# Kernel optimization log

Hardware: AMD Instinct MI355X
Metric: run time of the kernel (lower is better)

## Reference

```python
import jax, jax.numpy as jnp
import numpy as np

NUM_HEADS = 16
H_DIM = 1024
HEAD_DIM = H_DIM // NUM_HEADS  # 64
B, S = 8, 1024


def setup_inputs() -> dict:
    key = jax.random.key(0)
    ks = jax.random.split(key, 8)
    query = jax.random.normal(ks[0], (B, S, H_DIM), dtype=jnp.float32)
    key_t = jax.random.normal(ks[1], (B, S, H_DIM), dtype=jnp.float32)
    value = jax.random.normal(ks[2], (B, S, H_DIM), dtype=jnp.float32)
    attn_mask = jnp.ones((B, S, S), dtype=jnp.int32)
    # Per-head projection weights, stacked: [H, h_dim, head_dim]
    sc = 1.0 / np.sqrt(H_DIM)
    Wq = jax.random.normal(ks[3], (NUM_HEADS, H_DIM, HEAD_DIM), dtype=jnp.float32) * sc
    Wk = jax.random.normal(ks[4], (NUM_HEADS, H_DIM, HEAD_DIM), dtype=jnp.float32) * sc
    Wv = jax.random.normal(ks[5], (NUM_HEADS, H_DIM, HEAD_DIM), dtype=jnp.float32) * sc
    Wo = jax.random.normal(ks[6], (H_DIM, H_DIM), dtype=jnp.float32) * sc
    return {"query": query, "key": key_t, "value": value, "attn_mask": attn_mask,
            "Wq": Wq, "Wk": Wk, "Wv": Wv, "Wo": Wo}


def reference(query, key, value, attn_mask, Wq, Wk, Wv, Wo):
    scale = 1.0 / jnp.sqrt(jnp.float32(HEAD_DIM))  # from DotProductAttention.build
    # Fused per-head projections: [B,S,D] x [H,D,K] -> [B,H,S,K]
    q = jnp.einsum('bsd,hdk->bhsk', query, Wq)
    k = jnp.einsum('bsd,hdk->bhsk', key, Wk)
    v = jnp.einsum('bsd,hdk->bhsk', value, Wv)
    # Scores [B,H,S,S]; masked_fill where mask==0 (applied before scaling,
    # matching original; -inf * scale stays -inf)
    score = jnp.einsum('bhqk,bhmk->bhqm', q, k)
    mask = attn_mask[:, None, :, :]  # broadcast over heads
    score = jnp.where(mask == 0, -jnp.inf, score)
    p = jax.nn.softmax(score * scale, axis=-1)
    head = jnp.einsum('bhqm,bhmk->bhqk', p, v)  # [B,H,S,K]
    # Concat heads along feature dim: [B,S,H*K]
    concat = head.transpose(0, 2, 1, 3).reshape(B, S, H_DIM)
    return concat @ Wo
```

## Files before the change

kernel.cpp:

```cpp
#include <hip/hip_runtime.h>
#include <stdint.h>


typedef unsigned short u16;
typedef __attribute__((ext_vector_type(8))) short bf16x8;
typedef __attribute__((ext_vector_type(4))) float f32x4;
typedef __attribute__((ext_vector_type(4))) short short4_t;

#define MFMA16(a, b, c) __builtin_amdgcn_mfma_f32_16x16x32_bf16((a), (b), (c), 0, 0, 0)

__device__ __forceinline__ u16 f2bf(float f) {
  union { float f; uint32_t u; } v; v.f = f;
  uint32_t r = v.u + 0x7fffu + ((v.u >> 16) & 1u);
  return (u16)(r >> 16);
}
__device__ __forceinline__ u16 f2bf_fast(float f) {
  union { float f; uint32_t u; } v; v.f = f;
  return (u16)((v.u + 0x8000u) >> 16);
}

__device__ __forceinline__ void async16(const void* g, void* l) {
  __builtin_amdgcn_global_load_lds(
      (const __attribute__((address_space(1))) void*)g,
      (__attribute__((address_space(3))) void*)l, 16, 0, 0);
}

__device__ __forceinline__ void gemm_core(u16* As, u16* Bs, const u16* A,
                                          const u16* Bt, u16* C, float* Cf,
                                          int m0, int n0, int mode) {
  const int tid = threadIdx.x;
  const int lane = tid & 63;
  const int w = tid >> 6;
  const int wm = w >> 1, wn = w & 1;
  const int m_l = lane & 15;
  const int quad = lane >> 4;

  f32x4 acc[4][4];
#pragma unroll
  for (int i = 0; i < 4; i++)
#pragma unroll
    for (int j = 0; j < 4; j++) acc[i][j] = (f32x4){0.f, 0.f, 0.f, 0.f};

  const int rB = lane >> 2;
  const int cB = (((lane & 3) ^ ((rB >> 1) & 3))) * 8;
  const u16* a0 = A + (size_t)(m0 + (2 * w + 0) * 16 + rB) * 1024 + cB;
  const u16* a1 = A + (size_t)(m0 + (2 * w + 1) * 16 + rB) * 1024 + cB;
  const u16* b0 = Bt + (size_t)(n0 + (2 * w + 0) * 16 + rB) * 1024 + cB;
  const u16* b1 = Bt + (size_t)(n0 + (2 * w + 1) * 16 + rB) * 1024 + cB;
  u16* as0 = &As[(2 * w + 0) * 512];
  u16* as1 = &As[(2 * w + 1) * 512];
  u16* bs0 = &Bs[(2 * w + 0) * 512];
  u16* bs1 = &Bs[(2 * w + 1) * 512];

  for (int k0 = 0; k0 < 1024; k0 += 32) {
    __syncthreads();
    async16(a0 + k0, as0);
    async16(a1 + k0, as1);
    async16(b0 + k0, bs0);
    async16(b1 + k0, bs1);
    __syncthreads();

    bf16x8 af[4], bfr[4];
#pragma unroll
    for (int mt = 0; mt < 4; mt++) {
      int row = wm * 64 + mt * 16 + m_l;
      af[mt] =
          *(const bf16x8*)&As[row * 32 + (quad ^ ((m_l >> 1) & 3)) * 8];
    }
#pragma unroll
    for (int nt = 0; nt < 4; nt++) {
      int row = wn * 64 + nt * 16 + m_l;
      bfr[nt] =
          *(const bf16x8*)&Bs[row * 32 + (quad ^ ((m_l >> 1) & 3)) * 8];
    }
#pragma unroll
    for (int mt = 0; mt < 4; mt++)
#pragma unroll
      for (int nt = 0; nt < 4; nt++)
        acc[mt][nt] = MFMA16(af[mt], bfr[nt], acc[mt][nt]);
  }

#pragma unroll
  for (int mt = 0; mt < 4; mt++) {
    int m_base = m0 + wm * 64 + mt * 16 + quad * 4;
    int b = m_base >> 10, s = m_base & 1023;
#pragma unroll
    for (int nt = 0; nt < 4; nt++) {
      int n_g = n0 + wn * 64 + nt * 16 + m_l;
      if (mode == 0) {
        int h = n_g >> 6, d = n_g & 63;
        u16* p = C + ((size_t)(b * 16 + h) * 1024 + s) * 64 + d;
#pragma unroll
        for (int r = 0; r < 4; r++) p[(size_t)r * 64] = f2bf(acc[mt][nt][r]);
      } else if (mode == 1) {
        int h = n_g >> 6, d = n_g & 63;
        u16* p = C + ((size_t)(b * 16 + h) * 64 + d) * 1024 + s;
        short4_t pk;
#pragma unroll
        for (int r = 0; r < 4; r++) pk[r] = (short)f2bf(acc[mt][nt][r]);
        *(short4_t*)p = pk;
      } else {
        float* p = Cf + (size_t)m_base * 1024 + n_g;
#pragma unroll
        for (int r = 0; r < 4; r++) p[(size_t)r * 1024] = acc[mt][nt][r];
      }
    }
  }
}

__global__ __launch_bounds__(256) void qkv_kernel(
    const u16* __restrict__ q, const u16* __restrict__ k,
    const u16* __restrict__ v, const u16* __restrict__ wtq,
    const u16* __restrict__ wtk, const u16* __restrict__ wtv, u16* qb,
    u16* kb, u16* vt) {
  __shared__ u16 As[128 * 32], Bs[128 * 32];
  int z = blockIdx.z;
  const u16* A = (z == 0) ? q : (z == 1) ? k : v;
  const u16* Bt = (z == 0) ? wtq : (z == 1) ? wtk : wtv;
  u16* C = (z == 0) ? qb : (z == 1) ? kb : vt;
  gemm_core(As, Bs, A, Bt, C, nullptr, blockIdx.x * 128, blockIdx.y * 128,
            (z == 2) ? 1 : 0);
}

__global__ __launch_bounds__(256) void out_kernel(const u16* __restrict__ cc,
                                                  const u16* __restrict__ wto,
                                                  float* out) {
  __shared__ u16 As[128 * 32], Bs[128 * 32];
  gemm_core(As, Bs, cc, wto, nullptr, out, blockIdx.x * 128,
            blockIdx.y * 128, 2);
}

__global__ void conv_kernel(const float* __restrict__ q,
                            const float* __restrict__ k,
                            const float* __restrict__ v, u16* qc, u16* kc,
                            u16* vc) {
  int z = blockIdx.y;
  size_t t = ((size_t)blockIdx.x * 256 + threadIdx.x) * 4;
  const float* src = (z == 0) ? q : (z == 1) ? k : v;
  u16* dst = (z == 0) ? qc : (z == 1) ? kc : vc;
  float4 f = *(const float4*)(src + t);
  short4_t o;
  o[0] = (short)f2bf(f.x);
  o[1] = (short)f2bf(f.y);
  o[2] = (short)f2bf(f.z);
  o[3] = (short)f2bf(f.w);
  *(short4_t*)(dst + t) = o;
}

__global__ __launch_bounds__(256) void repack_t_kernel(
    const float* __restrict__ Wq, const float* __restrict__ Wk,
    const float* __restrict__ Wv, u16* wtq, u16* wtk, u16* wtv) {
  __shared__ u16 Ts[64 * 66];
  const int h = blockIdx.x, kkt = blockIdx.y, z = blockIdx.z;
  const float* W = (z == 0) ? Wq : (z == 1) ? Wk : Wv;
  u16* O = (z == 0) ? wtq : (z == 1) ? wtk : wtv;
  const int w = threadIdx.x >> 6, lane = threadIdx.x & 63;
#pragma unroll
  for (int i = 0; i < 16; i++) {
    int rr = i * 4 + w;
    float v = W[((size_t)h << 16) + (size_t)(kkt * 64 + rr) * 64 + lane];
    Ts[lane * 66 + rr] = f2bf(v);
  }
  __syncthreads();
#pragma unroll
  for (int i = 0; i < 16; i++) {
    int d = i * 4 + w;
    O[(size_t)(h * 64 + d) * 1024 + kkt * 64 + lane] = Ts[d * 66 + lane];
  }
}

__global__ void repack_wo_kernel(const float* __restrict__ Wo, u16* wto) {
  int t = blockIdx.x * 256 + threadIdx.x;
  int n = t >> 10, kk = t & 1023;
  wto[t] = f2bf(Wo[(kk << 10) + n]);
}

__global__ void pack_mask_kernel(const int* __restrict__ mask,
                                 uint32_t* __restrict__ bits) {
  int t = blockIdx.x * 256 + threadIdx.x;
  unsigned long long bal = __ballot(mask[t] != 0);
  if ((threadIdx.x & 63) == 0) {
    bits[t >> 5] = (uint32_t)bal;
    bits[(t >> 5) + 1] = (uint32_t)(bal >> 32);
  }
}

__global__ __launch_bounds__(256) void attn_kernel(
    const u16* __restrict__ qb, const u16* __restrict__ kb,
    const u16* __restrict__ vt, const uint32_t* __restrict__ mbits,
    u16* __restrict__ cc) {
  __shared__ u16 Ks[64 * 64];
  __shared__ u16 Vs[64 * 64];
  __shared__ u16 Ps[4][32 * 72];

  const int lane = threadIdx.x & 63;
  const int w = threadIdx.x >> 6;
  const int col = lane & 15;
  const int quad = lane >> 4;
  const int h = blockIdx.x, qt = blockIdx.y, b = blockIdx.z;
  const int q0 = qt * 128 + w * 32;
  const size_t bh = (size_t)b * 16 + h;

  const u16* qrow = qb + ((bh << 10) + q0 + col) * 64 + quad * 8;
  bf16x8 qa0 = *(const bf16x8*)qrow;
  bf16x8 qa1 = *(const bf16x8*)(qrow + 32);
  bf16x8 qb0 = *(const bf16x8*)(qrow + 16 * 64);
  bf16x8 qb1 = *(const bf16x8*)(qrow + 16 * 64 + 32);

  const u16* kbase = kb + (bh << 10) * 64;
  const u16* vbase = vt + (bh << 6) * 1024;
  const uint32_t* mrA = mbits + ((size_t)b * 1024 + q0 + col) * 32;
  const uint32_t* mrB = mrA + 16 * 32;
  u16* pwA = Ps[w];
  u16* pwB = Ps[w] + 16 * 72;

  const int LB0 = w * 64, LB1 = (4 + w) * 64;
  const int rS0 = (LB0 + lane) >> 3, cS0 = (lane & 7) ^ (rS0 & 7);
  const int rS1 = (LB1 + lane) >> 3, cS1 = (lane & 7) ^ (rS1 & 7);
  const int sw = col & 7;

  f32x4 O[2][4];
#pragma unroll
  for (int i = 0; i < 2; i++)
#pragma unroll
    for (int j = 0; j < 4; j++) O[i][j] = (f32x4){0.f, 0.f, 0.f, 0.f};
  float vsA = 0.f, vsB = 0.f;
  const float Cs = 0.18033688f;

  for (int kt = 0; kt < 1024; kt += 64) {
    __syncthreads();
    async16(kbase + (size_t)(kt + rS0) * 64 + cS0 * 8, &Ks[LB0 * 8]);
    async16(kbase + (size_t)(kt + rS1) * 64 + cS1 * 8, &Ks[LB1 * 8]);
    async16(vbase + (size_t)rS0 * 1024 + kt + cS0 * 8, &Vs[LB0 * 8]);
    async16(vbase + (size_t)rS1 * 1024 + kt + cS1 * 8, &Vs[LB1 * 8]);
    uint32_t mA0 = mrA[kt >> 5], mA1 = mrA[(kt >> 5) + 1];
    uint32_t mB0 = mrB[kt >> 5], mB1 = mrB[(kt >> 5) + 1];
    __syncthreads();

    bool allset = __all((mA0 & mA1 & mB0 & mB1) == 0xFFFFFFFFu);

#pragma unroll
    for (int st = 0; st < 4; st++) {
      const int krow = st * 16 + col;
      bf16x8 kf0 = *(const bf16x8*)&Ks[krow * 64 + (quad ^ sw) * 8];
      bf16x8 kf1 = *(const bf16x8*)&Ks[krow * 64 + ((4 + quad) ^ sw) * 8];
      const f32x4 z4 = {0.f, 0.f, 0.f, 0.f};
      f32x4 cA = MFMA16(kf0, qa0, z4); cA = MFMA16(kf1, qa1, cA);
      f32x4 cB = MFMA16(kf0, qb0, z4); cB = MFMA16(kf1, qb1, cB);

      float pa[4], pb[4];
#pragma unroll
      for (int r = 0; r < 4; r++) {
        pa[r] = __builtin_amdgcn_exp2f(cA[r] * Cs);
        pb[r] = __builtin_amdgcn_exp2f(cB[r] * Cs);
      }
      if (!allset) {
        uint32_t mwA = (st < 2) ? mA0 : mA1;
        uint32_t mwB = (st < 2) ? mB0 : mB1;
#pragma unroll
        for (int r = 0; r < 4; r++) {
          int bit = (st & 1) * 16 + quad * 4 + r;
          if (!((mwA >> bit) & 1u)) pa[r] = 0.f;
          if (!((mwB >> bit) & 1u)) pb[r] = 0.f;
        }
      }
      short4_t sa, sb;
#pragma unroll
      for (int r = 0; r < 4; r++) {
        vsA += pa[r];
        vsB += pb[r];
        sa[r] = (short)f2bf_fast(pa[r]);
        sb[r] = (short)f2bf_fast(pb[r]);
      }
      *(short4_t*)&pwA[col * 72 + st * 16 + quad * 4] = sa;
      *(short4_t*)&pwB[col * 72 + st * 16 + quad * 4] = sb;
    }

#pragma unroll
    for (int step = 0; step < 2; step++) {
      bf16x8 pfA = *(const bf16x8*)&pwA[col * 72 + step * 32 + quad * 8];
      bf16x8 pfB = *(const bf16x8*)&pwB[col * 72 + step * 32 + quad * 8];
#pragma unroll
      for (int dt = 0; dt < 4; dt++) {
        bf16x8 vf = *(const bf16x8*)&Vs[(dt * 16 + col) * 64 +
                                        ((step * 4 + quad) ^ sw) * 8];
        O[0][dt] = MFMA16(pfA, vf, O[0][dt]);
        O[1][dt] = MFMA16(pfB, vf, O[1][dt]);
      }
    }
  }

  vsA += __shfl_xor(vsA, 16); vsA += __shfl_xor(vsA, 32);
  vsB += __shfl_xor(vsB, 16); vsB += __shfl_xor(vsB, 32);
  float liA[4], liB[4];
#pragma unroll
  for (int r = 0; r < 4; r++) {
    liA[r] = 1.f / __shfl(vsA, quad * 4 + r);
    liB[r] = 1.f / __shfl(vsB, quad * 4 + r);
  }
  u16* crow = cc + ((size_t)b * 1024 + q0) * 1024 + h * 64;
#pragma unroll
  for (int dt = 0; dt < 4; dt++)
#pragma unroll
    for (int r = 0; r < 4; r++) {
      crow[(size_t)(quad * 4 + r) * 1024 + dt * 16 + col] =
          f2bf(O[0][dt][r] * liA[r]);
      crow[(size_t)(16 + quad * 4 + r) * 1024 + dt * 16 + col] =
          f2bf(O[1][dt][r] * liB[r]);
    }
}

extern "C" void kernel_launch(void* const* d_in, const int* in_sizes, int n_in,
                              void* d_out, int out_size, void* d_ws,
                              size_t ws_size, hipStream_t stream) {
  const float* query = (const float*)d_in[0];
  const float* key = (const float*)d_in[1];
  const float* value = (const float*)d_in[2];
  const int* mask = (const int*)d_in[3];
  const float* Wq = (const float*)d_in[4];
  const float* Wk = (const float*)d_in[5];
  const float* Wv = (const float*)d_in[6];
  const float* Wo = (const float*)d_in[7];
  float* out = (float*)d_out;

  u16* wtq = (u16*)d_ws;
  u16* wtk = wtq + (1 << 20);
  u16* wtv = wtk + (1 << 20);
  u16* wto = wtv + (1 << 20);
  u16* qc = wto + (1 << 20);
  u16* kc = qc + (8 << 20);
  u16* vc = kc + (8 << 20);
  u16* qbuf = vc + (8 << 20);
  u16* kbuf = qbuf + (8 << 20);
  u16* vtb = kbuf + (8 << 20);
  uint32_t* mbits = (uint32_t*)(vtb + (8 << 20));
  u16* ccb = qc;

  repack_t_kernel<<<dim3(16, 16, 3), 256, 0, stream>>>(Wq, Wk, Wv, wtq, wtk,
                                                       wtv);
  repack_wo_kernel<<<dim3(4096), 256, 0, stream>>>(Wo, wto);
  conv_kernel<<<dim3(8192, 3), 256, 0, stream>>>(query, key, value, qc, kc,
                                                 vc);
  pack_mask_kernel<<<dim3(32768), 256, 0, stream>>>(mask, mbits);
  qkv_kernel<<<dim3(64, 8, 3), 256, 0, stream>>>(qc, kc, vc, wtq, wtk, wtv,
                                                 qbuf, kbuf, vtb);
  attn_kernel<<<dim3(16, 8, 8), 256, 0, stream>>>(qbuf, kbuf, vtb, mbits, ccb);
  out_kernel<<<dim3(64, 8), 256, 0, stream>>>(ccb, wto, out);
}
```

Measured before the change: 350.0 us.

## Double-buffer LDS tiles in GEMM and attention, merge prep kernels into one

The GEMM core and the attention kernel now keep two shared-memory buffers. The next K/V or A/B tile is fetched asynchronously while the current one is consumed, which removes one barrier per iteration and overlaps global loads with MFMA work. The four preprocessing kernels (input conversion, weight repacks, mask packing) are merged into a single launch that dispatches on block index. Mask packing is rewritten to read 8 ints per thread with vector loads and emit one byte each. The trade-off is doubled LDS use, which may lower occupancy.

After: 328.1 us. -6.3%, faster.

```diff
diff --git a/kernel.cpp b/kernel.cpp
--- a/kernel.cpp
+++ b/kernel.cpp
@@ -47,37 +47,41 @@
   const u16* a1 = A + (size_t)(m0 + (2 * w + 1) * 16 + rB) * 1024 + cB;
   const u16* b0 = Bt + (size_t)(n0 + (2 * w + 0) * 16 + rB) * 1024 + cB;
   const u16* b1 = Bt + (size_t)(n0 + (2 * w + 1) * 16 + rB) * 1024 + cB;
-  u16* as0 = &As[(2 * w + 0) * 512];
-  u16* as1 = &As[(2 * w + 1) * 512];
-  u16* bs0 = &Bs[(2 * w + 0) * 512];
-  u16* bs1 = &Bs[(2 * w + 1) * 512];
+
+  auto stage = [&](int buf, int k0) {
+    async16(a0 + k0, &As[buf * 4096 + (2 * w + 0) * 512]);
+    async16(a1 + k0, &As[buf * 4096 + (2 * w + 1) * 512]);
+    async16(b0 + k0, &Bs[buf * 4096 + (2 * w + 0) * 512]);
+    async16(b1 + k0, &Bs[buf * 4096 + (2 * w + 1) * 512]);
+  };
+
+  stage(0, 0);
+  __syncthreads();
 
   for (int k0 = 0; k0 < 1024; k0 += 32) {
-    __syncthreads();
-    async16(a0 + k0, as0);
-    async16(a1 + k0, as1);
-    async16(b0 + k0, bs0);
-    async16(b1 + k0, bs1);
-    __syncthreads();
+    const int bb = (k0 >> 5) & 1;
+    if (k0 + 32 < 1024) stage(bb ^ 1, k0 + 32);
 
     bf16x8 af[4], bfr[4];
 #pragma unroll
     for (int mt = 0; mt < 4; mt++) {
       int row = wm * 64 + mt * 16 + m_l;
-      af[mt] =
-          *(const bf16x8*)&As[row * 32 + (quad ^ ((m_l >> 1) & 3)) * 8];
+      af[mt] = *(const bf16x8*)&As[bb * 4096 + row * 32 +
+                                   (quad ^ ((m_l >> 1) & 3)) * 8];
     }
 #pragma unroll
     for (int nt = 0; nt < 4; nt++) {
       int row = wn * 64 + nt * 16 + m_l;
-      bfr[nt] =
-          *(const bf16x8*)&Bs[row * 32 + (quad ^ ((m_l >> 1) & 3)) * 8];
+      bfr[nt] = *(const bf16x8*)&Bs[bb * 4096 + row * 32 +
+                                    (quad ^ ((m_l >> 1) & 3)) * 8];
     }
 #pragma unroll
     for (int mt = 0; mt < 4; mt++)
 #pragma unroll
       for (int nt = 0; nt < 4; nt++)
         acc[mt][nt] = MFMA16(af[mt], bfr[nt], acc[mt][nt]);
+
+    __syncthreads();
   }
 
 #pragma unroll
@@ -113,7 +117,7 @@
     const u16* __restrict__ v, const u16* __restrict__ wtq,
     const u16* __restrict__ wtk, const u16* __restrict__ wtv, u16* qb,
     u16* kb, u16* vt) {
-  __shared__ u16 As[128 * 32], Bs[128 * 32];
+  __shared__ u16 As[2 * 128 * 32], Bs[2 * 128 * 32];
   int z = blockIdx.z;
   const u16* A = (z == 0) ? q : (z == 1) ? k : v;
   const u16* Bt = (z == 0) ? wtq : (z == 1) ? wtk : wtv;
@@ -125,63 +129,73 @@
 __global__ __launch_bounds__(256) void out_kernel(const u16* __restrict__ cc,
                                                   const u16* __restrict__ wto,
                                                   float* out) {
-  __shared__ u16 As[128 * 32], Bs[128 * 32];
+  __shared__ u16 As[2 * 128 * 32], Bs[2 * 128 * 32];
   gemm_core(As, Bs, cc, wto, nullptr, out, blockIdx.x * 128,
             blockIdx.y * 128, 2);
 }
 
-__global__ void conv_kernel(const float* __restrict__ q,
-                            const float* __restrict__ k,
-                            const float* __restrict__ v, u16* qc, u16* kc,
-                            u16* vc) {
-  int z = blockIdx.y;
-  size_t t = ((size_t)blockIdx.x * 256 + threadIdx.x) * 4;
-  const float* src = (z == 0) ? q : (z == 1) ? k : v;
-  u16* dst = (z == 0) ? qc : (z == 1) ? kc : vc;
-  float4 f = *(const float4*)(src + t);
-  short4_t o;
-  o[0] = (short)f2bf(f.x);
-  o[1] = (short)f2bf(f.y);
-  o[2] = (short)f2bf(f.z);
-  o[3] = (short)f2bf(f.w);
-  *(short4_t*)(dst + t) = o;
-}
-
-__global__ __launch_bounds__(256) void repack_t_kernel(
-    const float* __restrict__ Wq, const float* __restrict__ Wk,
-    const float* __restrict__ Wv, u16* wtq, u16* wtk, u16* wtv) {
+#define PREP_CONV 24576
+#define PREP_RT (PREP_CONV + 768)
+#define PREP_WO (PREP_RT + 4096)
+#define PREP_MASK (PREP_WO + 4096)
+__global__ __launch_bounds__(256) void prep_kernel(
+    const float* __restrict__ q, const float* __restrict__ k,
+    const float* __restrict__ v, const float* __restrict__ Wq,
+    const float* __restrict__ Wk, const float* __restrict__ Wv,
+    const float* __restrict__ Wo, const int* __restrict__ mask, u16* qc,
+    u16* kc, u16* vc, u16* wtq, u16* wtk, u16* wtv, u16* wto,
+    uint32_t* __restrict__ mbits) {
   __shared__ u16 Ts[64 * 66];
-  const int h = blockIdx.x, kkt = blockIdx.y, z = blockIdx.z;
-  const float* W = (z == 0) ? Wq : (z == 1) ? Wk : Wv;
-  u16* O = (z == 0) ? wtq : (z == 1) ? wtk : wtv;
-  const int w = threadIdx.x >> 6, lane = threadIdx.x & 63;
-#pragma unroll
-  for (int i = 0; i < 16; i++) {
-    int rr = i * 4 + w;
-    float v = W[((size_t)h << 16) + (size_t)(kkt * 64 + rr) * 64 + lane];
-    Ts[lane * 66 + rr] = f2bf(v);
-  }
-  __syncthreads();
-#pragma unroll
-  for (int i = 0; i < 16; i++) {
-    int d = i * 4 + w;
-    O[(size_t)(h * 64 + d) * 1024 + kkt * 64 + lane] = Ts[d * 66 + lane];
-  }
-}
-
-__global__ void repack_wo_kernel(const float* __restrict__ Wo, u16* wto) {
-  int t = blockIdx.x * 256 + threadIdx.x;
-  int n = t >> 10, kk = t & 1023;
-  wto[t] = f2bf(Wo[(kk << 10) + n]);
-}
-
-__global__ void pack_mask_kernel(const int* __restrict__ mask,
-                                 uint32_t* __restrict__ bits) {
-  int t = blockIdx.x * 256 + threadIdx.x;
-  unsigned long long bal = __ballot(mask[t] != 0);
-  if ((threadIdx.x & 63) == 0) {
-    bits[t >> 5] = (uint32_t)bal;
-    bits[(t >> 5) + 1] = (uint32_t)(bal >> 32);
+  const int bid = blockIdx.x;
+  if (bid < PREP_CONV) {
+    int z = bid / 8192, i = bid - z * 8192;
+    size_t t = ((size_t)i * 256 + threadIdx.x) * 4;
+    const float* src = (z == 0) ? q : (z == 1) ? k : v;
+    u16* dst = (z == 0) ? qc : (z == 1) ? kc : vc;
+    float4 f = *(const float4*)(src + t);
+    short4_t o;
+    o[0] = (short)f2bf(f.x);
+    o[1] = (short)f2bf(f.y);
+    o[2] = (short)f2bf(f.z);
+    o[3] = (short)f2bf(f.w);
+    *(short4_t*)(dst + t) = o;
+  } else if (bid < PREP_RT) {
+    int idx = bid - PREP_CONV;
+    const int h = idx & 15, kkt = (idx >> 4) & 15, z = idx >> 8;
+    const float* W = (z == 0) ? Wq : (z == 1) ? Wk : Wv;
+    u16* O = (z == 0) ? wtq : (z == 1) ? wtk : wtv;
+    const int w = threadIdx.x >> 6, lane = threadIdx.x & 63;
+#pragma unroll
+    for (int i = 0; i < 16; i++) {
+      int rr = i * 4 + w;
+      float vv = W[((size_t)h << 16) + (size_t)(kkt * 64 + rr) * 64 + lane];
+      Ts[lane * 66 + rr] = f2bf(vv);
+    }
+    __syncthreads();
+#pragma unroll
+    for (int i = 0; i < 16; i++) {
+      int d = i * 4 + w;
+      O[(size_t)(h * 64 + d) * 1024 + kkt * 64 + lane] = Ts[d * 66 + lane];
+    }
+  } else if (bid < PREP_WO) {
+    int t = (bid - PREP_RT) * 256 + threadIdx.x;
+    int n = t >> 10, kk = t & 1023;
+    wto[t] = f2bf(Wo[(kk << 10) + n]);
+  } else {
+    int t = (bid - PREP_WO) * 256 + threadIdx.x;
+    const int* mp = mask + (size_t)t * 8;
+    int4 m0 = *(const int4*)mp;
+    int4 m1 = *(const int4*)(mp + 4);
+    uint32_t byte = 0;
+    byte |= (m0.x != 0) << 0;
+    byte |= (m0.y != 0) << 1;
+    byte |= (m0.z != 0) << 2;
+    byte |= (m0.w != 0) << 3;
+    byte |= (m1.x != 0) << 4;
+    byte |= (m1.y != 0) << 5;
+    byte |= (m1.z != 0) << 6;
+    byte |= (m1.w != 0) << 7;
+    ((uint8_t*)mbits)[t] = (uint8_t)byte;
   }
 }
 
@@ -189,8 +203,8 @@
     const u16* __restrict__ qb, const u16* __restrict__ kb,
     const u16* __restrict__ vt, const uint32_t* __restrict__ mbits,
     u16* __restrict__ cc) {
-  __shared__ u16 Ks[64 * 64];
-  __shared__ u16 Vs[64 * 64];
+  __shared__ u16 Ks[2][64 * 64];
+  __shared__ u16 Vs[2][64 * 64];
   __shared__ u16 Ps[4][32 * 72];
 
   const int lane = threadIdx.x & 63;
@@ -219,6 +233,13 @@
   const int rS1 = (LB1 + lane) >> 3, cS1 = (lane & 7) ^ (rS1 & 7);
   const int sw = col & 7;
 
+  auto stageKV = [&](int buf, int kt) {
+    async16(kbase + (size_t)(kt + rS0) * 64 + cS0 * 8, &Ks[buf][LB0 * 8]);
+    async16(kbase + (size_t)(kt + rS1) * 64 + cS1 * 8, &Ks[buf][LB1 * 8]);
+    async16(vbase + (size_t)rS0 * 1024 + kt + cS0 * 8, &Vs[buf][LB0 * 8]);
+    async16(vbase + (size_t)rS1 * 1024 + kt + cS1 * 8, &Vs[buf][LB1 * 8]);
+  };
+
   f32x4 O[2][4];
 #pragma unroll
   for (int i = 0; i < 2; i++)
@@ -227,23 +248,22 @@
   float vsA = 0.f, vsB = 0.f;
   const float Cs = 0.18033688f;
 
+  stageKV(0, 0);
+  __syncthreads();
+
   for (int kt = 0; kt < 1024; kt += 64) {
-    __syncthreads();
-    async16(kbase + (size_t)(kt + rS0) * 64 + cS0 * 8, &Ks[LB0 * 8]);
-    async16(kbase + (size_t)(kt + rS1) * 64 + cS1 * 8, &Ks[LB1 * 8]);
-    async16(vbase + (size_t)rS0 * 1024 + kt + cS0 * 8, &Vs[LB0 * 8]);
-    async16(vbase + (size_t)rS1 * 1024 + kt + cS1 * 8, &Vs[LB1 * 8]);
+    const int bb = (kt >> 6) & 1;
+    if (kt + 64 < 1024) stageKV(bb ^ 1, kt + 64);
+
     uint32_t mA0 = mrA[kt >> 5], mA1 = mrA[(kt >> 5) + 1];
     uint32_t mB0 = mrB[kt >> 5], mB1 = mrB[(kt >> 5) + 1];
-    __syncthreads();
-
     bool allset = __all((mA0 & mA1 & mB0 & mB1) == 0xFFFFFFFFu);
 
 #pragma unroll
     for (int st = 0; st < 4; st++) {
       const int krow = st * 16 + col;
-      bf16x8 kf0 = *(const bf16x8*)&Ks[krow * 64 + (quad ^ sw) * 8];
-      bf16x8 kf1 = *(const bf16x8*)&Ks[krow * 64 + ((4 + quad) ^ sw) * 8];
+      bf16x8 kf0 = *(const bf16x8*)&Ks[bb][krow * 64 + (quad ^ sw) * 8];
+      bf16x8 kf1 = *(const bf16x8*)&Ks[bb][krow * 64 + ((4 + quad) ^ sw) * 8];
       const f32x4 z4 = {0.f, 0.f, 0.f, 0.f};
       f32x4 cA = MFMA16(kf0, qa0, z4); cA = MFMA16(kf1, qa1, cA);
       f32x4 cB = MFMA16(kf0, qb0, z4); cB = MFMA16(kf1, qb1, cB);
@@ -282,12 +302,14 @@
       bf16x8 pfB = *(const bf16x8*)&pwB[col * 72 + step * 32 + quad * 8];
 #pragma unroll
       for (int dt = 0; dt < 4; dt++) {
-        bf16x8 vf = *(const bf16x8*)&Vs[(dt * 16 + col) * 64 +
-                                        ((step * 4 + quad) ^ sw) * 8];
+        bf16x8 vf = *(const bf16x8*)&Vs[bb][(dt * 16 + col) * 64 +
+                                           ((step * 4 + quad) ^ sw) * 8];
         O[0][dt] = MFMA16(pfA, vf, O[0][dt]);
         O[1][dt] = MFMA16(pfB, vf, O[1][dt]);
       }
     }
+
+    __syncthreads();
   }
 
   vsA += __shfl_xor(vsA, 16); vsA += __shfl_xor(vsA, 32);
@@ -336,12 +358,9 @@
   uint32_t* mbits = (uint32_t*)(vtb + (8 << 20));
   u16* ccb = qc;
 
-  repack_t_kernel<<<dim3(16, 16, 3), 256, 0, stream>>>(Wq, Wk, Wv, wtq, wtk,
-                                                       wtv);
-  repack_wo_kernel<<<dim3(4096), 256, 0, stream>>>(Wo, wto);
-  conv_kernel<<<dim3(8192, 3), 256, 0, stream>>>(query, key, value, qc, kc,
-                                                 vc);
-  pack_mask_kernel<<<dim3(32768), 256, 0, stream>>>(mask, mbits);
+  prep_kernel<<<dim3(PREP_MASK), 256, 0, stream>>>(
+      query, key, value, Wq, Wk, Wv, Wo, mask, qc, kc, vc, wtq, wtk, wtv, wto,
+      mbits);
   qkv_kernel<<<dim3(64, 8, 3), 256, 0, stream>>>(qc, kc, vc, wtq, wtk, wtv,
                                                  qbuf, kbuf, vtb);
   attn_kernel<<<dim3(16, 8, 8), 256, 0, stream>>>(qbuf, kbuf, vtb, mbits, ccb);
```
